# Kernel optimization log

Hardware: AMD Instinct MI355X
Metric: run time of the kernel (lower is better)

The kernel has to match this reference:

```python
import jax, jax.numpy as jnp
import numpy as np

D_MODEL = 2048
N_HEADS = 16
KV_HEADS = 4
HEAD_DIM = D_MODEL // N_HEADS            # 128
GROUP = N_HEADS // KV_HEADS              # 4
KV_WIDTH = KV_HEADS * HEAD_DIM           # 512
B, T = 2, 2048


def setup_inputs() -> dict:
    key = jax.random.key(0)
    ks = jax.random.split(key, 5)
    s = 0.02
    x = jax.random.normal(ks[0], (B, T, D_MODEL), dtype=jnp.float32)
    attn_mask = jnp.tril(jnp.ones((T, T), dtype=bool))  # causal
    qkv_w = jax.random.normal(ks[1], (D_MODEL, D_MODEL + 2 * KV_WIDTH), dtype=jnp.float32) * s
    qkv_b = jax.random.normal(ks[2], (D_MODEL + 2 * KV_WIDTH,), dtype=jnp.float32) * s
    proj_w = jax.random.normal(ks[3], (D_MODEL, D_MODEL), dtype=jnp.float32) * s
    proj_b = jax.random.normal(ks[4], (D_MODEL,), dtype=jnp.float32) * s
    return {"x": x, "attn_mask": attn_mask, "qkv_w": qkv_w, "qkv_b": qkv_b,
            "proj_w": proj_w, "proj_b": proj_b}


def reference(x, attn_mask, qkv_w, qkv_b, proj_w, proj_b):
    b, t, c = x.shape
    qkv = x @ qkv_w + qkv_b                               # [b,t,3072]
    q = qkv[..., :D_MODEL]
    k = qkv[..., D_MODEL:D_MODEL + KV_WIDTH]
    v = qkv[..., D_MODEL + KV_WIDTH:]
    # q: [b, kv_heads, group, t, d]; k,v: [b, kv_heads, t, d]
    q = q.reshape(b, t, KV_HEADS, GROUP, HEAD_DIM).transpose(0, 2, 3, 1, 4)
    k = k.reshape(b, t, KV_HEADS, HEAD_DIM).transpose(0, 2, 1, 3)
    v = v.reshape(b, t, KV_HEADS, HEAD_DIM).transpose(0, 2, 1, 3)
    scale = 1.0 / jnp.sqrt(jnp.asarray(HEAD_DIM, dtype=x.dtype))
    att = jnp.einsum('bkgtd,bksd->bkgts', q, k) * scale   # [b,kv,g,t,t]
    att = jnp.where(attn_mask, att, jnp.asarray(-jnp.inf, dtype=att.dtype))
    att = jax.nn.softmax(att, axis=-1)
    out = jnp.einsum('bkgts,bksd->bkgtd', att, v)         # [b,kv,g,t,d]
    out = out.transpose(0, 3, 1, 2, 4).reshape(b, t, c)
    return out @ proj_w + proj_b
```

## Files before the change

### kernel.cpp

```cpp
#include <hip/hip_runtime.h>
#include <cstdint>
#include <cstddef>

#define D_MODEL 2048
#define T_SEQ   2048
#define BATCH   2
#define N_HEADS 16
#define KV_HEADS 4
#define HEAD_DIM 128
#define QKV_N   3072
#define ROWS    (BATCH * T_SEQ)

typedef float  floatx4 __attribute__((ext_vector_type(4)));
typedef short  shortx8 __attribute__((ext_vector_type(8)));
typedef __bf16 bf16x8  __attribute__((ext_vector_type(8)));

typedef const void __attribute__((address_space(1))) gvoid_t;
typedef void __attribute__((address_space(3)))       svoid_t;

__device__ __forceinline__ floatx4 mfma16(shortx8 a, shortx8 b, floatx4 c) {
  return __builtin_amdgcn_mfma_f32_16x16x32_bf16(
      __builtin_bit_cast(bf16x8, a), __builtin_bit_cast(bf16x8, b), c, 0, 0, 0);
}

__device__ __forceinline__ unsigned short f2bf(float f) {
  union { float f; unsigned int u; } v; v.f = f;
  unsigned int u = v.u;
  u += 0x7fffu + ((u >> 16) & 1u);
  return (unsigned short)(u >> 16);
}

__device__ __forceinline__ unsigned short f2bf_hw(float f) {
  return __builtin_bit_cast(unsigned short, (__bf16)f);
}

__global__ void cvt_x(const float* __restrict__ in, unsigned short* __restrict__ out, int n4) {
  int i = blockIdx.x * blockDim.x + threadIdx.x;
  if (i >= n4) return;
  float4 v = ((const float4*)in)[i];
  ushort4 o;
  o.x = f2bf(v.x); o.y = f2bf(v.y); o.z = f2bf(v.z); o.w = f2bf(v.w);
  ((ushort4*)out)[i] = o;
}

__global__ void transpose_cvt(const float* __restrict__ W, unsigned short* __restrict__ Wt,
                              int K, int N) {
  __shared__ float tile[32][33];
  int n0 = blockIdx.x * 32, k0 = blockIdx.y * 32;
  int tx = threadIdx.x, ty = threadIdx.y;
  #pragma unroll
  for (int i = 0; i < 32; i += 8)
    tile[ty + i][tx] = W[(size_t)(k0 + ty + i) * N + n0 + tx];
  __syncthreads();
  #pragma unroll
  for (int i = 0; i < 32; i += 8)
    Wt[(size_t)(n0 + ty + i) * K + k0 + tx] = f2bf(tile[tx][ty + i]);
}

__global__ void build_kt(const unsigned short* __restrict__ qkv, unsigned short* __restrict__ kst) {
  int o = blockIdx.x * blockDim.x + threadIdx.x;
  int t   = o & 2047;
  int d8  = (o >> 11) & 15;
  int kvh = (o >> 15) & 3;
  int b   = o >> 17;
  uint4 v = *(const uint4*)(qkv + (size_t)(b * T_SEQ + t) * QKV_N
                            + D_MODEL + kvh * HEAD_DIM + d8 * 8);
  *(uint4*)(kst + (size_t)o * 8) = v;
}

__global__ void build_vt(const unsigned short* __restrict__ qkv, unsigned short* __restrict__ vst) {
  int o = blockIdx.x * blockDim.x + threadIdx.x;
  int d   = o & 127;
  int t8  = (o >> 7) & 255;
  int kvh = (o >> 15) & 3;
  int b   = o >> 17;
  const unsigned short* src = qkv + (size_t)(b * T_SEQ + t8 * 8) * QKV_N
                              + D_MODEL + 512 + kvh * HEAD_DIM + d;
  union { unsigned short s[8]; uint4 v; } tmp;
  #pragma unroll
  for (int j = 0; j < 8; ++j) tmp.s[j] = src[(size_t)j * QKV_N];
  *(uint4*)(vst + (size_t)o * 8) = tmp.v;
}

template<int NB>
__global__ __launch_bounds__(512, 2) void gemm256(
    const unsigned short* __restrict__ A,
    const unsigned short* __restrict__ Bt,
    const float* __restrict__ bias,
    void* __restrict__ Cout,
    int M, int N, int K, int c_bf16)
{
  __shared__ __align__(16) unsigned short lds[32768 + NB * 16384];
  const int tid  = threadIdx.x;
  const int wave = tid >> 6, lane = tid & 63;
  const int quad = lane >> 4, l16 = lane & 15;
  const int wr = wave >> 2, wc = wave & 3;
  const int bm = blockIdx.y * 256, bn = blockIdx.x * (NB * 128);
  const int NT = K >> 6;

  const int r0 = tid >> 3;
  const int cx = (tid & 7) ^ (r0 & 7);
  const size_t K64 = (size_t)64 * K;
  const unsigned short* a_src = A  + (size_t)(bm + r0) * K + cx * 8;
  const unsigned short* b_src = Bt + (size_t)(bn + r0) * K + cx * 8;
  const int wOff = wave * 512;

  #define LDSA_(buf, half) (lds + (((buf) << 1) + (half)) * 8192)
  #define LDSB_(buf, half) (lds + 32768 + (((buf) << 1) + (half)) * (NB * 4096))
  #define KOFFA(h, t) ((size_t)(h) * 128 * K + (size_t)(t) * 64)
  #define KOFFB(h, t) ((size_t)(h) * (64 * NB) * K + (size_t)(t) * 64)
  #define STAGE_A(srcbase, ldshalf, koff) do {                                        \
    __builtin_amdgcn_global_load_lds((gvoid_t*)((srcbase) + (koff)),                  \
        (svoid_t*)((ldshalf) + wOff), 16, 0, 0);                                      \
    __builtin_amdgcn_global_load_lds((gvoid_t*)((srcbase) + (koff) + K64),            \
        (svoid_t*)((ldshalf) + wOff + 4096), 16, 0, 0);                               \
  } while (0)
  #define STAGE_B(srcbase, ldshalf, koff) do {                                        \
    _Pragma("unroll")                                                                 \
    for (int j_ = 0; j_ < NB; ++j_)                                                   \
      __builtin_amdgcn_global_load_lds(                                               \
          (gvoid_t*)((srcbase) + (koff) + (size_t)j_ * K64),                          \
          (svoid_t*)((ldshalf) + wOff + j_ * 4096), 16, 0, 0);                        \
  } while (0)

  const int rowA = (wr * 64 + l16) * 64;
  const int rowB = (wc * (16 * NB) + l16) * 64;
  const int xo0 = ((quad)     ^ (l16 & 7)) * 8;
  const int xo1 = ((4 + quad) ^ (l16 & 7)) * 8;

  floatx4 acc[8][2 * NB] = {};
  shortx8 Afr[4][2];
  shortx8 Bfr[2 * NB][2];

  STAGE_A(a_src, LDSA_(0, 0), KOFFA(0, 0));
  STAGE_B(b_src, LDSB_(0, 0), KOFFB(0, 0));
  STAGE_B(b_src, LDSB_(0, 1), KOFFB(1, 0));
  STAGE_A(a_src, LDSA_(0, 1), KOFFA(1, 0));
  if (NT > 1) {
    STAGE_A(a_src, LDSA_(1, 0), KOFFA(0, 1));
    STAGE_B(b_src, LDSB_(1, 0), KOFFB(0, 1));
    STAGE_B(b_src, LDSB_(1, 1), KOFFB(1, 1));
  }

  for (int t = 0; t < NT; ++t) {
    const int buf = t & 1;
    unsigned short* sA0 = LDSA_(buf, 0);
    unsigned short* sA1 = LDSA_(buf, 1);
    unsigned short* sB0 = LDSB_(buf, 0);
    unsigned short* sB1 = LDSB_(buf, 1);

    if (t == NT - 1) asm volatile("s_waitcnt vmcnt(0)" ::: "memory");
    else if constexpr (NB == 2) asm volatile("s_waitcnt vmcnt(6)" ::: "memory");
    else                        asm volatile("s_waitcnt vmcnt(4)" ::: "memory");
    __builtin_amdgcn_s_barrier();
    #pragma unroll
    for (int mi = 0; mi < 4; ++mi) {
      Afr[mi][0] = *(const shortx8*)(sA0 + rowA + mi * 1024 + xo0);
      Afr[mi][1] = *(const shortx8*)(sA0 + rowA + mi * 1024 + xo1);
    }
    #pragma unroll
    for (int ni = 0; ni < NB; ++ni) {
      Bfr[ni][0] = *(const shortx8*)(sB0 + rowB + ni * 1024 + xo0);
      Bfr[ni][1] = *(const shortx8*)(sB0 + rowB + ni * 1024 + xo1);
    }
    if (t + 1 < NT) STAGE_A(a_src, LDSA_(buf ^ 1, 1), KOFFA(1, t + 1));
    asm volatile("s_waitcnt lgkmcnt(0)" ::: "memory");
    __builtin_amdgcn_s_setprio(1);
    #pragma unroll
    for (int ks = 0; ks < 2; ++ks)
      #pragma unroll
      for (int mi = 0; mi < 4; ++mi)
        #pragma unroll
        for (int ni = 0; ni < NB; ++ni)
          acc[mi][ni] = mfma16(Afr[mi][ks], Bfr[ni][ks], acc[mi][ni]);
    __builtin_amdgcn_s_setprio(0);
    __builtin_amdgcn_s_barrier();

    #pragma unroll
    for (int ni = 0; ni < NB; ++ni) {
      Bfr[NB + ni][0] = *(const shortx8*)(sB1 + rowB + ni * 1024 + xo0);
      Bfr[NB + ni][1] = *(const shortx8*)(sB1 + rowB + ni * 1024 + xo1);
    }
    if (t + 2 < NT) STAGE_A(a_src, LDSA_(buf, 0), KOFFA(0, t + 2));
    __builtin_amdgcn_s_barrier();
    asm volatile("s_waitcnt lgkmcnt(0)" ::: "memory");
    __builtin_amdgcn_s_setprio(1);
    #pragma unroll
    for (int ks = 0; ks < 2; ++ks)
      #pragma unroll
      for (int mi = 0; mi < 4; ++mi)
        #pragma unroll
        for (int ni = 0; ni < NB; ++ni)
          acc[mi][NB + ni] = mfma16(Afr[mi][ks], Bfr[NB + ni][ks], acc[mi][NB + ni]);
    __builtin_amdgcn_s_setprio(0);
    __builtin_amdgcn_s_barrier();

    #pragma unroll
    for (int mi = 0; mi < 4; ++mi) {
      Afr[mi][0] = *(const shortx8*)(sA1 + rowA + mi * 1024 + xo0);
      Afr[mi][1] = *(const shortx8*)(sA1 + rowA + mi * 1024 + xo1);
    }
    if (t + 2 < NT) STAGE_B(b_src, LDSB_(buf, 0), KOFFB(0, t + 2));
    __builtin_amdgcn_s_barrier();
    asm volatile("s_waitcnt lgkmcnt(0)" ::: "memory");
    __builtin_amdgcn_s_setprio(1);
    #pragma unroll
    for (int ks = 0; ks < 2; ++ks)
      #pragma unroll
      for (int mi = 0; mi < 4; ++mi)
        #pragma unroll
        for (int ni = 0; ni < NB; ++ni)
          acc[4 + mi][NB + ni] = mfma16(Afr[mi][ks], Bfr[NB + ni][ks], acc[4 + mi][NB + ni]);
    __builtin_amdgcn_s_setprio(0);
    __builtin_amdgcn_s_barrier();

    if (t + 2 < NT) STAGE_B(b_src, LDSB_(buf, 1), KOFFB(1, t + 2));
    __builtin_amdgcn_s_barrier();
    __builtin_amdgcn_s_setprio(1);
    #pragma unroll
    for (int ks = 0; ks < 2; ++ks)
      #pragma unroll
      for (int mi = 0; mi < 4; ++mi)
        #pragma unroll
        for (int ni = 0; ni < NB; ++ni)
          acc[4 + mi][ni] = mfma16(Afr[mi][ks], Bfr[ni][ks], acc[4 + mi][ni]);
    __builtin_amdgcn_s_setprio(0);
    __builtin_amdgcn_s_barrier();
  }

  #pragma unroll
  for (int mi = 0; mi < 8; ++mi) {
    const int row = bm + (mi >> 2) * 128 + wr * 64 + (mi & 3) * 16 + quad * 4;
    #pragma unroll
    for (int ni = 0; ni < 2 * NB; ++ni) {
      const int col = bn + (ni / NB) * (64 * NB) + wc * (16 * NB) + (ni % NB) * 16 + l16;
      const float bv = bias[col];
      #pragma unroll
      for (int r = 0; r < 4; ++r) {
        float v = acc[mi][ni][r] + bv;
        if (c_bf16)
          ((unsigned short*)Cout)[(size_t)(row + r) * N + col] = f2bf_hw(v);
        else
          ((float*)Cout)[(size_t)(row + r) * N + col] = v;
      }
    }
  }
  #undef LDSA_
  #undef LDSB_
  #undef KOFFA
  #undef KOFFB
  #undef STAGE_A
  #undef STAGE_B
}

__global__ __launch_bounds__(512, 4) void attn_kernel(
    const unsigned short* __restrict__ qkv,
    const unsigned short* __restrict__ kst,
    const unsigned short* __restrict__ vst,
    unsigned short* __restrict__ aout)
{
  __shared__ __align__(16) unsigned short sK[2][16 * 64 * 8];
  __shared__ __align__(16) unsigned short sV[2][8 * 128 * 8];
  __shared__ __align__(16) unsigned short sP[8][4 * 16 * 8];

  const int tid  = threadIdx.x;
  const int wave = tid >> 6, lane = tid & 63;
  const int split = wave >> 2, g = wave & 3;
  const int quad = lane >> 4, l16 = lane & 15;
  const int head = blockIdx.y, b = blockIdx.z;
  const int kvh = head >> 2;
  const float cf = 0.08838834764831845f * 1.4426950408889634f;
  const float THR = 25.0f;

  const unsigned short* kbase = kst + (size_t)((b * KV_HEADS + kvh) * 16) * 2048 * 8;
  const unsigned short* vbase = vst + (size_t)((b * KV_HEADS + kvh) * 256) * 128 * 8;
  unsigned short* sPw = sP[wave];

  float* mrgO  = (float*)&sK[0][0];
  float* mrgML = (float*)&sV[0][0];

  #define STAGE_KV(sp, kb_) do {                                               \
    _Pragma("unroll")                                                          \
    for (int it_ = 0; it_ < 4; ++it_) {                                        \
      const int c_ = it_ * 4 + g;                                              \
      __builtin_amdgcn_global_load_lds(                                        \
          (gvoid_t*)(kbase + ((size_t)c_ * 2048 + (kb_)) * 8 + lane * 8),      \
          (svoid_t*)(&sK[sp][c_ * 512]), 16, 0, 0);                            \
    }                                                                          \
    const unsigned short* vt_ = vbase + (size_t)((kb_) >> 3) * 128 * 8;        \
    _Pragma("unroll")                                                          \
    for (int it_ = 0; it_ < 4; ++it_) {                                        \
      const int c_ = it_ * 4 + g;                                              \
      __builtin_amdgcn_global_load_lds(                                        \
          (gvoid_t*)(vt_ + c_ * 512 + lane * 8),                               \
          (svoid_t*)(&sV[sp][c_ * 512]), 16, 0, 0);                            \
    }                                                                          \
  } while (0)

  #pragma unroll 1
  for (int half = 0; half < 2; ++half) {
    const int qt = half ? blockIdx.x : (31 - blockIdx.x);
    const int q0 = qt * 64;

    shortx8 qf[4];
    {
      const unsigned short* qp = qkv + (size_t)(b * T_SEQ + q0 + g * 16 + l16) * QKV_N
                                 + head * HEAD_DIM + quad * 8;
      #pragma unroll
      for (int ks = 0; ks < 4; ++ks)
        qf[ks] = *(const shortx8*)(qp + ks * 32);
    }

    float m_i[4], l_i[4];
    #pragma unroll
    for (int r = 0; r < 4; ++r) { m_i[r] = -__builtin_inff(); l_i[r] = 0.f; }
    floatx4 o_acc[8] = {};

    const int J = (qt >> 1) + 1;
    for (int j = 0; j < J; ++j) {
      const int kt = 2 * j + split;
      const bool act = (kt <= qt);
      floatx4 s[4] = {};

      __builtin_amdgcn_s_barrier();
      if (act) STAGE_KV(split, kt * 64);
      asm volatile("s_waitcnt vmcnt(4)" ::: "memory");
      __builtin_amdgcn_s_barrier();

      if (act) {
        __builtin_amdgcn_s_setprio(1);
        #pragma unroll
        for (int ks = 0; ks < 4; ++ks) {
          #pragma unroll
          for (int ct = 0; ct < 4; ++ct) {
            shortx8 kf = *(const shortx8*)&sK[split][((ks * 4 + quad) * 64 + ct * 16 + l16) * 8];
            s[ct] = mfma16(qf[ks], kf, s[ct]);
          }
        }
        __builtin_amdgcn_s_setprio(0);

        if (kt == qt) {
          const int qrow = q0 + g * 16 + quad * 4;
          const int kb = kt * 64;
          #pragma unroll
          for (int ct = 0; ct < 4; ++ct) {
            const int kcol = kb + ct * 16 + l16;
            #pragma unroll
            for (int r = 0; r < 4; ++r)
              if (kcol > qrow + r) s[ct][r] = -__builtin_inff();
          }
        }

        float lmx[4];
        bool over = false;
        #pragma unroll
        for (int r = 0; r < 4; ++r) {
          lmx[r] = fmaxf(fmaxf(s[0][r], s[1][r]), fmaxf(s[2][r], s[3][r]));
          over = over || (lmx[r] > m_i[r] + THR);
        }
        if (__ballot(over)) {
          float alpha_r[4];
          #pragma unroll
          for (int r = 0; r < 4; ++r) {
            float m = lmx[r];
            m = fmaxf(m, __shfl_xor(m, 1));
            m = fmaxf(m, __shfl_xor(m, 2));
            m = fmaxf(m, __shfl_xor(m, 4));
            m = fmaxf(m, __shfl_xor(m, 8));
            const float newm = fmaxf(m_i[r], m);
            alpha_r[r] = exp2f((m_i[r] - newm) * cf);
            m_i[r] = newm;
            l_i[r] *= alpha_r[r];
          }
          #pragma unroll
          for (int nt = 0; nt < 8; ++nt)
            #pragma unroll
            for (int r = 0; r < 4; ++r) o_acc[nt][r] *= alpha_r[r];
        }

        #pragma unroll
        for (int r = 0; r < 4; ++r) {
          const float nmc = m_i[r] * cf;
          float p0 = exp2f(fmaf(s[0][r], cf, -nmc));
          float p1 = exp2f(fmaf(s[1][r], cf, -nmc));
          float p2 = exp2f(fmaf(s[2][r], cf, -nmc));
          float p3 = exp2f(fmaf(s[3][r], cf, -nmc));
          s[0][r] = p0; s[1][r] = p1; s[2][r] = p2; s[3][r] = p3;
          l_i[r] += (p0 + p1) + (p2 + p3);
        }
      }

      asm volatile("s_waitcnt vmcnt(0)" ::: "memory");
      __builtin_amdgcn_s_barrier();

      if (act) {
        #pragma unroll
        for (int c = 0; c < 2; ++c) {
          #pragma unroll
          for (int ctl = 0; ctl < 2; ++ctl) {
            const int ct = c * 2 + ctl;
            #pragma unroll
            for (int r = 0; r < 4; ++r)
              sPw[((ctl * 2 + (l16 >> 3)) * 16 + quad * 4 + r) * 8 + (l16 & 7)] =
                  f2bf_hw(s[ct][r]);
          }
          __asm__ __volatile__("s_waitcnt lgkmcnt(0)" ::: "memory");
          shortx8 pf = *(const shortx8*)&sPw[(quad * 16 + l16) * 8];
          __builtin_amdgcn_s_setprio(1);
          #pragma unroll
          for (int nt = 0; nt < 8; ++nt) {
            shortx8 vf = *(const shortx8*)&sV[split][((c * 4 + quad) * 128 + nt * 16 + l16) * 8];
            o_acc[nt] = mfma16(pf, vf, o_acc[nt]);
          }
          __builtin_amdgcn_s_setprio(0);
        }
      }
    }

    __builtin_amdgcn_s_barrier();
    if (split == 1) {
      #pragma unroll
      for (int nt = 0; nt < 8; ++nt)
        #pragma unroll
        for (int r = 0; r < 4; ++r)
          mrgO[g * 2048 + (quad * 4 + r) * 128 + nt * 16 + l16] = o_acc[nt][r];
      #pragma unroll
      for (int r = 0; r < 4; ++r) {
        mrgML[(g * 64 + lane) * 8 + r * 2]     = m_i[r];
        mrgML[(g * 64 + lane) * 8 + r * 2 + 1] = l_i[r];
      }
    }
    asm volatile("s_waitcnt lgkmcnt(0)" ::: "memory");
    __builtin_amdgcn_s_barrier();

    if (split == 0) {
      float lm[4], a0[4], a1[4];
      #pragma unroll
      for (int r = 0; r < 4; ++r) {
        const float m1 = mrgML[(g * 64 + lane) * 8 + r * 2];
        const float l1 = mrgML[(g * 64 + lane) * 8 + r * 2 + 1];
        const float M = fmaxf(m_i[r], m1);
        a0[r] = exp2f((m_i[r] - M) * cf);
        a1[r] = exp2f((m1 - M) * cf);
        lm[r] = a0[r] * l_i[r] + a1[r] * l1;
      }
      #pragma unroll
      for (int nt = 0; nt < 8; ++nt)
        #pragma unroll
        for (int r = 0; r < 4; ++r)
          o_acc[nt][r] = a0[r] * o_acc[nt][r]
                       + a1[r] * mrgO[g * 2048 + (quad * 4 + r) * 128 + nt * 16 + l16];

      const int trow = q0 + g * 16 + quad * 4;
      #pragma unroll
      for (int r = 0; r < 4; ++r) {
        float l = lm[r];
        l += __shfl_xor(l, 1);
        l += __shfl_xor(l, 2);
        l += __shfl_xor(l, 4);
        l += __shfl_xor(l, 8);
        const float inv = 1.f / l;
        #pragma unroll
        for (int nt = 0; nt < 8; ++nt) {
          aout[(size_t)(b * T_SEQ + trow + r) * D_MODEL + head * HEAD_DIM + nt * 16 + l16] =
              f2bf_hw(o_acc[nt][r] * inv);
        }
      }
    }
  }
  #undef STAGE_KV
}

extern "C" void kernel_launch(void* const* d_in, const int* in_sizes, int n_in,
                              void* d_out, int out_size, void* d_ws, size_t ws_size,
                              hipStream_t stream) {
  const float* x      = (const float*)d_in[0];
  const float* qkv_w  = (const float*)d_in[2];
  const float* qkv_b  = (const float*)d_in[3];
  const float* proj_w = (const float*)d_in[4];
  const float* proj_b = (const float*)d_in[5];
  float* out = (float*)d_out;

  char* ws = (char*)d_ws;
  unsigned short* x_bf    = (unsigned short*)(ws);
  unsigned short* qkvw_t  = (unsigned short*)(ws + (size_t)16777216);
  unsigned short* projw_t = (unsigned short*)(ws + (size_t)29360128);
  unsigned short* qkvbuf  = (unsigned short*)(ws + (size_t)37748736);
  unsigned short* vstaged = (unsigned short*)(ws + (size_t)62914560);
  unsigned short* kstaged = qkvw_t;
  unsigned short* attn_out = x_bf;

  cvt_x<<<(ROWS * D_MODEL / 4 + 255) / 256, 256, 0, stream>>>(x, x_bf, ROWS * D_MODEL / 4);
  transpose_cvt<<<dim3(QKV_N / 32, D_MODEL / 32), dim3(32, 8), 0, stream>>>(qkv_w, qkvw_t, D_MODEL, QKV_N);
  transpose_cvt<<<dim3(D_MODEL / 32, D_MODEL / 32), dim3(32, 8), 0, stream>>>(proj_w, projw_t, D_MODEL, D_MODEL);
  gemm256<2><<<dim3(QKV_N / 256, ROWS / 256), 512, 0, stream>>>(
      x_bf, qkvw_t, qkv_b, (void*)qkvbuf, ROWS, QKV_N, D_MODEL, 1);
  build_kt<<<1024, 256, 0, stream>>>(qkvbuf, kstaged);
  build_vt<<<1024, 256, 0, stream>>>(qkvbuf, vstaged);
  attn_kernel<<<dim3(16, N_HEADS, BATCH), 512, 0, stream>>>(qkvbuf, kstaged, vstaged, attn_out);
  gemm256<1><<<dim3(D_MODEL / 128, ROWS / 256), 512, 0, stream>>>(
      attn_out, projw_t, proj_b, (void*)out, ROWS, D_MODEL, D_MODEL, 0);
}
```

Before: 311.5 us.

## Fuse K/V staging into QKV GEMM epilogue and merge prep kernels

The QKV GEMM epilogue now writes Q to a compact buffer and scatters K and V straight into the staged layouts the attention kernel reads. This removes the separate build_kt/build_vt passes and the round trip through a full qkv buffer. The x conversion and both weight transposes are merged into one prep kernel to cut launch count. The cost is scattered 2-byte stores in the GEMM epilogue for the K/V columns, which may coalesce poorly.

```diff
diff --git a/kernel.cpp b/kernel.cpp
--- a/kernel.cpp
+++ b/kernel.cpp
@@ -34,20 +34,27 @@
   return __builtin_bit_cast(unsigned short, (__bf16)f);
 }
 
-__global__ void cvt_x(const float* __restrict__ in, unsigned short* __restrict__ out, int n4) {
-  int i = blockIdx.x * blockDim.x + threadIdx.x;
-  if (i >= n4) return;
-  float4 v = ((const float4*)in)[i];
-  ushort4 o;
-  o.x = f2bf(v.x); o.y = f2bf(v.y); o.z = f2bf(v.z); o.w = f2bf(v.w);
-  ((ushort4*)out)[i] = o;
-}
-
-__global__ void transpose_cvt(const float* __restrict__ W, unsigned short* __restrict__ Wt,
-                              int K, int N) {
+__global__ __launch_bounds__(256) void prep_kernel(
+    const float* __restrict__ x, unsigned short* __restrict__ x_bf,
+    const float* __restrict__ qkv_w, unsigned short* __restrict__ qkvw_t,
+    const float* __restrict__ proj_w, unsigned short* __restrict__ projw_t)
+{
   __shared__ float tile[32][33];
-  int n0 = blockIdx.x * 32, k0 = blockIdx.y * 32;
-  int tx = threadIdx.x, ty = threadIdx.y;
+  const int bid = blockIdx.x, tid = threadIdx.x;
+  if (bid < 8192) {
+    const int i = bid * 256 + tid;
+    float4 v = ((const float4*)x)[i];
+    ushort4 o;
+    o.x = f2bf(v.x); o.y = f2bf(v.y); o.z = f2bf(v.z); o.w = f2bf(v.w);
+    ((ushort4*)x_bf)[i] = o;
+    return;
+  }
+  const float* W; unsigned short* Wt; int N, bx, by;
+  if (bid < 14336) { const int v = bid - 8192;  W = qkv_w;  Wt = qkvw_t;  N = QKV_N;   bx = v % 96; by = v / 96; }
+  else             { const int v = bid - 14336; W = proj_w; Wt = projw_t; N = D_MODEL; bx = v % 64; by = v / 64; }
+  const int K = D_MODEL;
+  const int n0 = bx * 32, k0 = by * 32;
+  const int tx = tid & 31, ty = tid >> 5;
   #pragma unroll
   for (int i = 0; i < 32; i += 8)
     tile[ty + i][tx] = W[(size_t)(k0 + ty + i) * N + n0 + tx];
@@ -57,38 +64,15 @@
     Wt[(size_t)(n0 + ty + i) * K + k0 + tx] = f2bf(tile[tx][ty + i]);
 }
 
-__global__ void build_kt(const unsigned short* __restrict__ qkv, unsigned short* __restrict__ kst) {
-  int o = blockIdx.x * blockDim.x + threadIdx.x;
-  int t   = o & 2047;
-  int d8  = (o >> 11) & 15;
-  int kvh = (o >> 15) & 3;
-  int b   = o >> 17;
-  uint4 v = *(const uint4*)(qkv + (size_t)(b * T_SEQ + t) * QKV_N
-                            + D_MODEL + kvh * HEAD_DIM + d8 * 8);
-  *(uint4*)(kst + (size_t)o * 8) = v;
-}
-
-__global__ void build_vt(const unsigned short* __restrict__ qkv, unsigned short* __restrict__ vst) {
-  int o = blockIdx.x * blockDim.x + threadIdx.x;
-  int d   = o & 127;
-  int t8  = (o >> 7) & 255;
-  int kvh = (o >> 15) & 3;
-  int b   = o >> 17;
-  const unsigned short* src = qkv + (size_t)(b * T_SEQ + t8 * 8) * QKV_N
-                              + D_MODEL + 512 + kvh * HEAD_DIM + d;
-  union { unsigned short s[8]; uint4 v; } tmp;
-  #pragma unroll
-  for (int j = 0; j < 8; ++j) tmp.s[j] = src[(size_t)j * QKV_N];
-  *(uint4*)(vst + (size_t)o * 8) = tmp.v;
-}
-
 template<int NB>
 __global__ __launch_bounds__(512, 2) void gemm256(
     const unsigned short* __restrict__ A,
     const unsigned short* __restrict__ Bt,
     const float* __restrict__ bias,
     void* __restrict__ Cout,
-    int M, int N, int K, int c_bf16)
+    unsigned short* __restrict__ kst,
+    unsigned short* __restrict__ vst,
+    int M, int N, int K, int cmode)
 {
   __shared__ __align__(16) unsigned short lds[32768 + NB * 16384];
   const int tid  = threadIdx.x;
@@ -238,10 +222,22 @@
       #pragma unroll
       for (int r = 0; r < 4; ++r) {
         float v = acc[mi][ni][r] + bv;
-        if (c_bf16)
-          ((unsigned short*)Cout)[(size_t)(row + r) * N + col] = f2bf_hw(v);
-        else
+        if (cmode == 0) {
           ((float*)Cout)[(size_t)(row + r) * N + col] = v;
+        } else {
+          const unsigned short h = f2bf_hw(v);
+          const int rw = row + r;
+          const int t = rw & 2047, bb = rw >> 11;
+          if (col < 2048) {
+            ((unsigned short*)Cout)[(size_t)rw * 2048 + col] = h;
+          } else if (col < 2560) {
+            const int c2 = col - 2048, kvh = c2 >> 7, d = c2 & 127;
+            kst[((((size_t)bb * 4 + kvh) * 16 + (d >> 3)) * 2048 + t) * 8 + (d & 7)] = h;
+          } else {
+            const int c2 = col - 2560, kvh = c2 >> 7, d = c2 & 127;
+            vst[((((size_t)bb * 4 + kvh) * 256 + (t >> 3)) * 128 + d) * 8 + (t & 7)] = h;
+          }
+        }
       }
     }
   }
@@ -254,7 +250,7 @@
 }
 
 __global__ __launch_bounds__(512, 4) void attn_kernel(
-    const unsigned short* __restrict__ qkv,
+    const unsigned short* __restrict__ qbuf,
     const unsigned short* __restrict__ kst,
     const unsigned short* __restrict__ vst,
     unsigned short* __restrict__ aout)
@@ -304,7 +300,7 @@
 
     shortx8 qf[4];
     {
-      const unsigned short* qp = qkv + (size_t)(b * T_SEQ + q0 + g * 16 + l16) * QKV_N
+      const unsigned short* qp = qbuf + (size_t)(b * T_SEQ + q0 + g * 16 + l16) * 2048
                                  + head * HEAD_DIM + quad * 8;
       #pragma unroll
       for (int ks = 0; ks < 4; ++ks)
@@ -485,19 +481,15 @@
   unsigned short* x_bf    = (unsigned short*)(ws);
   unsigned short* qkvw_t  = (unsigned short*)(ws + (size_t)16777216);
   unsigned short* projw_t = (unsigned short*)(ws + (size_t)29360128);
-  unsigned short* qkvbuf  = (unsigned short*)(ws + (size_t)37748736);
-  unsigned short* vstaged = (unsigned short*)(ws + (size_t)62914560);
-  unsigned short* kstaged = qkvw_t;
+  unsigned short* qbuf    = (unsigned short*)(ws + (size_t)37748736);
+  unsigned short* kstaged = (unsigned short*)(ws + (size_t)54525952);
+  unsigned short* vstaged = (unsigned short*)(ws + (size_t)58720256);
   unsigned short* attn_out = x_bf;
 
-  cvt_x<<<(ROWS * D_MODEL / 4 + 255) / 256, 256, 0, stream>>>(x, x_bf, ROWS * D_MODEL / 4);
-  transpose_cvt<<<dim3(QKV_N / 32, D_MODEL / 32), dim3(32, 8), 0, stream>>>(qkv_w, qkvw_t, D_MODEL, QKV_N);
-  transpose_cvt<<<dim3(D_MODEL / 32, D_MODEL / 32), dim3(32, 8), 0, stream>>>(proj_w, projw_t, D_MODEL, D_MODEL);
+  prep_kernel<<<18432, 256, 0, stream>>>(x, x_bf, qkv_w, qkvw_t, proj_w, projw_t);
   gemm256<2><<<dim3(QKV_N / 256, ROWS / 256), 512, 0, stream>>>(
-      x_bf, qkvw_t, qkv_b, (void*)qkvbuf, ROWS, QKV_N, D_MODEL, 1);
-  build_kt<<<1024, 256, 0, stream>>>(qkvbuf, kstaged);
-  build_vt<<<1024, 256, 0, stream>>>(qkvbuf, vstaged);
-  attn_kernel<<<dim3(16, N_HEADS, BATCH), 512, 0, stream>>>(qkvbuf, kstaged, vstaged, attn_out);
+      x_bf, qkvw_t, qkv_b, (void*)qbuf, kstaged, vstaged, ROWS, QKV_N, D_MODEL, 2);
+  attn_kernel<<<dim3(16, N_HEADS, BATCH), 512, 0, stream>>>(qbuf, kstaged, vstaged, attn_out);
   gemm256<1><<<dim3(D_MODEL / 128, ROWS / 256), 512, 0, stream>>>(
-      attn_out, projw_t, proj_b, (void*)out, ROWS, D_MODEL, D_MODEL, 0);
-}
+      attn_out, projw_t, proj_b, (void*)out, nullptr, nullptr, ROWS, D_MODEL, D_MODEL, 0);
+}
```

Measured after the change: 313.9 us. No clear change (+0.8%).
